# Performance work log

Measured on AMD Instinct MI355X. Metric: run time of the kernel, lower is better.

## Reference

```python
import jax, jax.numpy as jnp
import numpy as np
from jax import lax

# retina / model config (matches init_kwargs)
G, K, S = 64, 3, 2            # first patch size, n scales, scale factor
B, C, H, W = 64, 3, 512, 512  # input batch
C1, C2 = 64, 128              # feature extractor channels


def setup_inputs() -> dict:
    key = jax.random.key(0)
    k1, k2, k3, k4 = jax.random.split(key, 4)
    x = jax.random.normal(k1, (B, C, H, W), jnp.float32)
    # normalized fixation coords in [-1, 1]
    l = jax.random.uniform(k2, (B, 2), jnp.float32, minval=-1.0, maxval=1.0)
    w1 = jax.random.normal(k3, (C1, C, 3, 3), jnp.float32) * 0.05
    b1 = jnp.zeros((C1,), jnp.float32)
    w2 = jax.random.normal(k4, (C2, C1, 3, 3), jnp.float32) * 0.05
    b2 = jnp.zeros((C2,), jnp.float32)
    return {"x": x, "l": l, "w1": w1, "b1": b1, "w2": w2, "b2": b2}


def _conv(x, w, stride):
    return lax.conv_general_dilated(
        x, w, (stride, stride), 'SAME',
        dimension_numbers=('NCHW', 'OIHW', 'NCHW'))


def _extract_patches(x, coords, size):
    """Batched equivalent of crude_retina.extract_patch.

    Torch pads by size//2+1 only when the crop exceeds the image; padding
    unconditionally and offsetting the start indices yields identical values.
    x: (B,C,H,W), coords: (B,2) int [y,x]. Returns (B,C,size,size).
    """
    pad = size // 2 + 1
    xp = jnp.pad(x, ((0, 0), (0, 0), (pad, pad), (pad, pad)))
    start_y = coords[:, 0] - size // 2 + pad
    start_x = coords[:, 1] - size // 2 + pad

    def slice_one(im, sy, sx):
        return lax.dynamic_slice(im, (0, sy, sx), (im.shape[0], size, size))

    return jax.vmap(slice_one)(xp, start_y, start_x)


def _resize_nearest(p, g):
    # torch F.interpolate(mode='nearest'): src = floor(dst * in/out)
    size = p.shape[-1]
    idx = (jnp.arange(g) * size) // g
    return p[:, :, idx][:, :, :, idx]


def reference(x, l, w1, b1, w2, b2):
    T = jnp.array([H, W], jnp.float32)
    # to_exocentric: floor(0.5*(l+1)*T) clamped to [0, max(H,W)]
    coords = jnp.clip(jnp.floor(0.5 * (l + 1.0) * T), 0, max(H, W)).astype(jnp.int32)

    # multi-scale foveation
    phi = []
    size = G
    for _ in range(K):
        p = _extract_patches(x, coords, size)
        if size != G:
            p = _resize_nearest(p, G)
        phi.append(p)
        size = int(S * size)
    phi = jnp.stack(phi, axis=1)  # (B, K, C, G, G)

    # feature extractor applied per patch scale
    outs = []
    for i in range(K):
        h = jax.nn.relu(_conv(phi[:, i], w1, 1) + b1[:, None, None])
        h = jax.nn.relu(_conv(h, w2, 2) + b2[:, None, None])
        outs.append(h)
    return jnp.stack(outs, axis=1)  # (B, K, C2, G//2, G//2)
```

## Files before the change

### kernel.cpp

```cpp
#include <hip/hip_runtime.h>
#include <hip/hip_bf16.h>

typedef __attribute__((ext_vector_type(4))) float  f32x4;
typedef __attribute__((ext_vector_type(8))) _Float16 f16x8;

#define LDA1 40

static __device__ __forceinline__ void gld_lds16(const void* g, void* l) {
    __builtin_amdgcn_global_load_lds(
        (const __attribute__((address_space(1))) void*)g,
        (__attribute__((address_space(3))) void*)l, 16, 0, 0);
}

__global__ void transform_kernel(const float* __restrict__ w1, const float* __restrict__ w2,
                                 _Float16* __restrict__ Bt1, _Float16* __restrict__ Bt2)
{
    const int i = blockIdx.x * 256 + threadIdx.x;
    if (i < 64 * 32) {
        const int n = i >> 5, k = i & 31;
        const float v = (k < 27) ? w1[n * 27 + k] : 0.0f;
        Bt1[i] = (_Float16)v;
    }
    const int j = i - 64 * 32;
    if (j >= 0 && j < 9 * 128 * 64) {
        const int tap = j / (128 * 64);
        const int rem = j % (128 * 64);
        const int n = rem >> 6;
        const int c1 = rem & 63;
        Bt2[j] = (_Float16)w2[((size_t)n * 64 + c1) * 9 + tap];
    }
}

__global__ __launch_bounds__(256) void conv1_mfma(
    const float* __restrict__ x, const float* __restrict__ l,
    const _Float16* __restrict__ Bt1, const float* __restrict__ b1,
    _Float16* __restrict__ h1, int bk0)
{
    const int img = blockIdx.y;
    const int bk  = bk0 + img;
    const int b   = bk / 3, ksc = bk % 3;
    const int step = 1 << ksc;
    const int half = 32 << ksc;
    const int py0 = blockIdx.x * 4;

    const float ly = l[b * 2 + 0], lx = l[b * 2 + 1];
    int cy = (int)floorf(0.5f * (ly + 1.0f) * 512.0f);
    int cx = (int)floorf(0.5f * (lx + 1.0f) * 512.0f);
    cy = min(max(cy, 0), 512);
    cx = min(max(cx, 0), 512);
    const int sy = cy - half, sx = cx - half;

    __shared__ float    patch[3 * 6 * 66];
    __shared__ _Float16 A_lds[256 * LDA1];
    __shared__ _Float16 out_t[256 * 64];

    const int t = threadIdx.x;
    const float* xb = x + (size_t)b * 3 * 512 * 512;
    for (int i = t; i < 3 * 6 * 66; i += 256) {
        const int c  = i / 396, r = i % 396;
        const int ry = r / 66, xx = r % 66;
        const int yy = py0 - 1 + ry;
        const int col = xx - 1;
        const int iy = sy + yy * step, ix = sx + col * step;
        float v = 0.0f;
        if (yy >= 0 && yy < 64 && col >= 0 && col < 64 &&
            iy >= 0 && iy < 512 && ix >= 0 && ix < 512)
            v = xb[(size_t)c * 262144 + iy * 512 + ix];
        patch[i] = v;
    }
    __syncthreads();

    {
        const int pyl = t >> 6, px = t & 63;
        _Float16* arow = &A_lds[t * LDA1];
        #pragma unroll
        for (int k = 0; k < 27; ++k) {
            const int c = k / 9, rr = k % 9, kh = rr / 3, kw = rr % 3;
            arow[k] = (_Float16)patch[c * 396 + (pyl + kh) * 66 + (px + kw)];
        }
        #pragma unroll
        for (int k = 27; k < 32; ++k) arow[k] = (_Float16)0.0f;
    }
    __syncthreads();

    const int wave = t >> 6, lane = t & 63;
    const int lrow = lane & 15, kb = lane >> 4;

    f16x8 bfr[4];
    #pragma unroll
    for (int nf = 0; nf < 4; ++nf)
        bfr[nf] = *(const f16x8*)(Bt1 + ((size_t)(nf * 16 + lrow)) * 32 + kb * 8);

    f32x4 acc[4][4];
    #pragma unroll
    for (int mf = 0; mf < 4; ++mf)
        #pragma unroll
        for (int nf = 0; nf < 4; ++nf)
            #pragma unroll
            for (int r = 0; r < 4; ++r) acc[mf][nf][r] = 0.0f;

    #pragma unroll
    for (int mf = 0; mf < 4; ++mf) {
        const f16x8 afr = *(const f16x8*)(&A_lds[((wave * 4 + mf) * 16 + lrow) * LDA1 + kb * 8]);
        #pragma unroll
        for (int nf = 0; nf < 4; ++nf)
            acc[mf][nf] = __builtin_amdgcn_mfma_f32_16x16x32_f16(afr, bfr[nf], acc[mf][nf], 0, 0, 0);
    }

    #pragma unroll
    for (int mf = 0; mf < 4; ++mf) {
        const int ml0 = (wave * 4 + mf) * 16 + kb * 4;
        #pragma unroll
        for (int nf = 0; nf < 4; ++nf) {
            const int c1 = nf * 16 + lrow;
            const float bb = b1[c1];
            #pragma unroll
            for (int r = 0; r < 4; ++r) {
                const float v = fmaxf(acc[mf][nf][r] + bb, 0.0f);
                const int ml = ml0 + r;
                const int xcol = ml & 63;
                const int psx = ((xcol & 1) << 5) | (xcol >> 1);
                const int pl  = (ml & ~63) | psx;
                const int c1s = c1 ^ ((psx & 7) << 3);
                out_t[pl * 64 + c1s] = (_Float16)v;
            }
        }
    }
    __syncthreads();

    _Float16* hb = h1 + (size_t)img * 4096 * 64 + (size_t)py0 * 64 * 64;
    #pragma unroll
    for (int j = 0; j < 8; ++j) {
        const int idx = j * 256 + t;
        *(f16x8*)(hb + (size_t)idx * 8) = *(const f16x8*)&out_t[idx * 8];
    }
}

__global__ __launch_bounds__(256) void conv2_mfma(
    const _Float16* __restrict__ h1, const _Float16* __restrict__ Bt2,
    const float* __restrict__ b2, float* __restrict__ out, int bk0)
{
    const int img = blockIdx.y;
    const int bk  = bk0 + img;
    const int mc  = blockIdx.x;
    const int t = threadIdx.x, wave = t >> 6, lane = t & 63;
    const int lrow = lane & 15, kb = lane >> 4;
    const int wq = wave >> 1;
    const int wn = wave & 1;

    __shared__ _Float16 As[5 * 4096 + 2 * 8192];
    _Float16* Bs = As + 5 * 4096;

    const _Float16* hb = h1 + (size_t)img * 4096 * 64;
    const int ys = mc * 4;
    const int nrows = (mc == 15) ? 4 : 5;

    if (mc == 15) {
        f16x8 z = {};
        *(f16x8*)&As[4 * 4096 + t * 16]     = z;
        *(f16x8*)&As[4 * 4096 + t * 16 + 8] = z;
    }

    {
        const _Float16* ga = hb + (size_t)ys * 4096;
        #pragma unroll
        for (int j = 0; j < 10; ++j) {
            if (j < nrows * 2) {
                const int c = j * 256 + t;
                gld_lds16(ga + (size_t)c * 8, As + (j * 256 + wave * 64) * 8);
            }
        }
    }
    {
        #pragma unroll
        for (int i = 0; i < 4; ++i) {
            const int c = i * 256 + t;
            const int r = c >> 3, j = c & 7;
            const int jt = j ^ (r & 7);
            gld_lds16(Bt2 + (size_t)r * 64 + jt * 8,
                      Bs + (i * 256 + wave * 64) * 8);
        }
    }

    f32x4 acc[2][4];
    #pragma unroll
    for (int mf = 0; mf < 2; ++mf)
        #pragma unroll
        for (int nf = 0; nf < 4; ++nf)
            #pragma unroll
            for (int r = 0; r < 4; ++r) acc[mf][nf][r] = 0.0f;

    #pragma unroll 1
    for (int tap = 0; tap < 9; ++tap) {
        __syncthreads();
        if (tap < 8) {
            const _Float16* gb = Bt2 + (size_t)(tap + 1) * 8192;
            const int slot = (tap + 1) & 1;
            #pragma unroll
            for (int i = 0; i < 4; ++i) {
                const int c = i * 256 + t;
                const int r = c >> 3, j = c & 7;
                const int jt = j ^ (r & 7);
                gld_lds16(gb + (size_t)r * 64 + jt * 8,
                          Bs + slot * 8192 + (i * 256 + wave * 64) * 8);
            }
        }
        const int kh = tap / 3, kw = tap % 3;
        const int par = kw & 1;
        const int rrow = 2 * wq + kh;
        const int slot = tap & 1;

        #pragma unroll
        for (int c1h = 0; c1h < 2; ++c1h) {
            const int jt = c1h * 4 + kb;
            f16x8 afr[2];
            #pragma unroll
            for (int mf = 0; mf < 2; ++mf) {
                const int ox = mf * 16 + lrow;
                const int xh = ox + (kw >> 1);
                const int p  = rrow * 64 + par * 32 + xh;
                f16x8 v = *(const f16x8*)&As[p * 64 + (jt ^ (p & 7)) * 8];
                if ((kw == 2) && (ox == 31)) v = (f16x8){};
                afr[mf] = v;
            }
            #pragma unroll
            for (int nf = 0; nf < 4; ++nf) {
                const int r = wn * 64 + nf * 16 + lrow;
                const f16x8 bfr = *(const f16x8*)&Bs[slot * 8192 + r * 64 + (jt ^ (r & 7)) * 8];
                #pragma unroll
                for (int mf = 0; mf < 2; ++mf)
                    acc[mf][nf] = __builtin_amdgcn_mfma_f32_16x16x32_f16(afr[mf], bfr, acc[mf][nf], 0, 0, 0);
            }
        }
    }

    float* ob = out + (size_t)bk * 128 * 1024;
    #pragma unroll
    for (int mf = 0; mf < 2; ++mf) {
        const int m0 = mc * 64 + wq * 32 + mf * 16 + kb * 4;
        #pragma unroll
        for (int nf = 0; nf < 4; ++nf) {
            const int c2 = wn * 64 + nf * 16 + lrow;
            const float bb = b2[c2];
            f32x4 v;
            #pragma unroll
            for (int r = 0; r < 4; ++r) v[r] = fmaxf(acc[mf][nf][r] + bb, 0.0f);
            *(f32x4*)(ob + (size_t)c2 * 1024 + m0) = v;
        }
    }
}

extern "C" void kernel_launch(void* const* d_in, const int* in_sizes, int n_in,
                              void* d_out, int out_size, void* d_ws, size_t ws_size,
                              hipStream_t stream) {
    const float* x  = (const float*)d_in[0];
    const float* l  = (const float*)d_in[1];
    const float* w1 = (const float*)d_in[2];
    const float* b1 = (const float*)d_in[3];
    const float* w2 = (const float*)d_in[4];
    const float* b2 = (const float*)d_in[5];
    float* out = (float*)d_out;

    _Float16* Bt1 = (_Float16*)d_ws;
    _Float16* Bt2 = Bt1 + 64 * 32;
    _Float16* h1  = (_Float16*)((char*)d_ws + 160 * 1024);

    const int total_imgs = 192;
    const size_t per_img = (size_t)4096 * 64 * sizeof(_Float16);
    size_t h1_cap = (ws_size > 160 * 1024) ? ws_size - 160 * 1024 : 0;
    int ipc = (int)(h1_cap / per_img);
    if (ipc > total_imgs) ipc = total_imgs;
    if (ipc < 1) ipc = 1;

    transform_kernel<<<296, 256, 0, stream>>>(w1, w2, Bt1, Bt2);

    for (int bk0 = 0; bk0 < total_imgs; bk0 += ipc) {
        const int n = (total_imgs - bk0 < ipc) ? (total_imgs - bk0) : ipc;
        conv1_mfma<<<dim3(16, n), 256, 0, stream>>>(x, l, Bt1, b1, h1, bk0);
        conv2_mfma<<<dim3(16, n), 256, 0, stream>>>(h1, Bt2, b2, out, bk0);
    }
}
```

Measured before the change: 102.6 us.

## Gather conv1 im2col fragments directly from global into MFMA registers

Conv1 no longer stages a float patch tile and an im2col matrix in LDS. Each lane gathers its 8 K-elements straight from global memory into the B fragment, using precomputed per-lane offsets. The MFMA is also transposed so each lane's outputs are 4 consecutive channels, written as packed f16x4 stores. Each block now handles 16 rows in four sub-iterations, with a quarter as many blocks, which cuts LDS traffic and barriers but gives fewer blocks and relies on the cache for overlapping gathers.

New measurement: 111.2 us. 8.4% more time.

```diff
diff --git a/kernel.cpp b/kernel.cpp
--- a/kernel.cpp
+++ b/kernel.cpp
@@ -3,8 +3,7 @@
 
 typedef __attribute__((ext_vector_type(4))) float  f32x4;
 typedef __attribute__((ext_vector_type(8))) _Float16 f16x8;
-
-#define LDA1 40
+typedef __attribute__((ext_vector_type(4))) _Float16 f16x4;
 
 static __device__ __forceinline__ void gld_lds16(const void* g, void* l) {
     __builtin_amdgcn_global_load_lds(
@@ -41,7 +40,12 @@
     const int b   = bk / 3, ksc = bk % 3;
     const int step = 1 << ksc;
     const int half = 32 << ksc;
-    const int py0 = blockIdx.x * 4;
+    const int quarter = blockIdx.x;
+
+    const int t = threadIdx.x, wave = t >> 6, lane = t & 63;
+    const int lrow = lane & 15, kb = lane >> 4;
+
+    __shared__ _Float16 out_t[256 * 64];
 
     const float ly = l[b * 2 + 0], lx = l[b * 2 + 1];
     int cy = (int)floorf(0.5f * (ly + 1.0f) * 512.0f);
@@ -50,89 +54,73 @@
     cx = min(max(cx, 0), 512);
     const int sy = cy - half, sx = cx - half;
 
-    __shared__ float    patch[3 * 6 * 66];
-    __shared__ _Float16 A_lds[256 * LDA1];
-    __shared__ _Float16 out_t[256 * 64];
-
-    const int t = threadIdx.x;
-    const float* xb = x + (size_t)b * 3 * 512 * 512;
-    for (int i = t; i < 3 * 6 * 66; i += 256) {
-        const int c  = i / 396, r = i % 396;
-        const int ry = r / 66, xx = r % 66;
-        const int yy = py0 - 1 + ry;
-        const int col = xx - 1;
-        const int iy = sy + yy * step, ix = sx + col * step;
-        float v = 0.0f;
-        if (yy >= 0 && yy < 64 && col >= 0 && col < 64 &&
-            iy >= 0 && iy < 512 && ix >= 0 && ix < 512)
-            v = xb[(size_t)c * 262144 + iy * 512 + ix];
-        patch[i] = v;
-    }
-    __syncthreads();
-
-    {
-        const int pyl = t >> 6, px = t & 63;
-        _Float16* arow = &A_lds[t * LDA1];
-        #pragma unroll
-        for (int k = 0; k < 27; ++k) {
-            const int c = k / 9, rr = k % 9, kh = rr / 3, kw = rr % 3;
-            arow[k] = (_Float16)patch[c * 396 + (pyl + kh) * 66 + (px + kw)];
-        }
-        #pragma unroll
-        for (int k = 27; k < 32; ++k) arow[k] = (_Float16)0.0f;
-    }
-    __syncthreads();
-
-    const int wave = t >> 6, lane = t & 63;
-    const int lrow = lane & 15, kb = lane >> 4;
-
-    f16x8 bfr[4];
-    #pragma unroll
-    for (int nf = 0; nf < 4; ++nf)
-        bfr[nf] = *(const f16x8*)(Bt1 + ((size_t)(nf * 16 + lrow)) * 32 + kb * 8);
-
-    f32x4 acc[4][4];
-    #pragma unroll
-    for (int mf = 0; mf < 4; ++mf)
-        #pragma unroll
-        for (int nf = 0; nf < 4; ++nf)
-            #pragma unroll
-            for (int r = 0; r < 4; ++r) acc[mf][nf][r] = 0.0f;
-
-    #pragma unroll
-    for (int mf = 0; mf < 4; ++mf) {
-        const f16x8 afr = *(const f16x8*)(&A_lds[((wave * 4 + mf) * 16 + lrow) * LDA1 + kb * 8]);
-        #pragma unroll
-        for (int nf = 0; nf < 4; ++nf)
-            acc[mf][nf] = __builtin_amdgcn_mfma_f32_16x16x32_f16(afr, bfr[nf], acc[mf][nf], 0, 0, 0);
-    }
-
-    #pragma unroll
-    for (int mf = 0; mf < 4; ++mf) {
-        const int ml0 = (wave * 4 + mf) * 16 + kb * 4;
-        #pragma unroll
-        for (int nf = 0; nf < 4; ++nf) {
-            const int c1 = nf * 16 + lrow;
-            const float bb = b1[c1];
-            #pragma unroll
-            for (int r = 0; r < 4; ++r) {
-                const float v = fmaxf(acc[mf][nf][r] + bb, 0.0f);
-                const int ml = ml0 + r;
-                const int xcol = ml & 63;
-                const int psx = ((xcol & 1) << 5) | (xcol >> 1);
-                const int pl  = (ml & ~63) | psx;
-                const int c1s = c1 ^ ((psx & 7) << 3);
-                out_t[pl * 64 + c1s] = (_Float16)v;
-            }
-        }
-    }
-    __syncthreads();
-
-    _Float16* hb = h1 + (size_t)img * 4096 * 64 + (size_t)py0 * 64 * 64;
+    f16x8 w1f[4];
+    f32x4 b1v[4];
+    #pragma unroll
+    for (int nf = 0; nf < 4; ++nf) {
+        w1f[nf] = *(const f16x8*)(Bt1 + ((size_t)(nf * 16 + lrow)) * 32 + kb * 8);
+        b1v[nf] = *(const f32x4*)(b1 + nf * 16 + kb * 4);
+    }
+
+    const int px = wave * 16 + lrow;
+    const float* xb = x + (size_t)b * 3 * 262144;
+    int dyj[8];
+    int ixoff[8];
     #pragma unroll
     for (int j = 0; j < 8; ++j) {
-        const int idx = j * 256 + t;
-        *(f16x8*)(hb + (size_t)idx * 8) = *(const f16x8*)&out_t[idx * 8];
+        const int k   = kb * 8 + j;
+        const int c   = (k * 57) >> 9;
+        const int rem = k - c * 9;
+        const int kh  = (rem * 43) >> 7;
+        const int kw  = rem - kh * 3;
+        const int xx  = px + kw - 1;
+        const int ix  = sx + xx * step;
+        const bool xok = (k < 27) && (xx >= 0) && (xx < 64) && (ix >= 0) && (ix < 512);
+        dyj[j]   = kh - 1;
+        ixoff[j] = xok ? (c * 262144 + ix) : -1;
+    }
+
+    const int psx = ((px & 1) << 5) | (px >> 1);
+    const int c1sb = ((psx & 7) << 3);
+
+    const int py0 = quarter * 16;
+    #pragma unroll 1
+    for (int sub = 0; sub < 4; ++sub) {
+        #pragma unroll
+        for (int il = 0; il < 4; ++il) {
+            const int py  = py0 + sub * 4 + il;
+            const int iyb = sy + py * step;
+            f16x8 pfr = {};
+            #pragma unroll
+            for (int j = 0; j < 8; ++j) {
+                const int yy = py + dyj[j];
+                const int iy = iyb + dyj[j] * step;
+                float v = 0.0f;
+                if (ixoff[j] >= 0 && yy >= 0 && yy < 64 && iy >= 0 && iy < 512)
+                    v = xb[(size_t)ixoff[j] + iy * 512];
+                pfr[j] = (_Float16)v;
+            }
+            f32x4 zero = {0.0f, 0.0f, 0.0f, 0.0f};
+            #pragma unroll
+            for (int nf = 0; nf < 4; ++nf) {
+                const f32x4 d = __builtin_amdgcn_mfma_f32_16x16x32_f16(w1f[nf], pfr, zero, 0, 0, 0);
+                f16x4 hv;
+                #pragma unroll
+                for (int r = 0; r < 4; ++r)
+                    hv[r] = (_Float16)fmaxf(d[r] + b1v[nf][r], 0.0f);
+                const int c1s = (nf * 16 + kb * 4) ^ c1sb;
+                *(f16x4*)&out_t[(il * 64 + psx) * 64 + c1s] = hv;
+            }
+        }
+        __syncthreads();
+        _Float16* hb = h1 + (size_t)img * 4096 * 64
+                          + (size_t)(quarter * 1024 + sub * 256) * 64;
+        #pragma unroll
+        for (int jj = 0; jj < 8; ++jj) {
+            const int idx = jj * 256 + t;
+            *(f16x8*)(hb + (size_t)idx * 8) = *(const f16x8*)&out_t[idx * 8];
+        }
+        __syncthreads();
     }
 }
 
@@ -276,7 +264,7 @@
 
     for (int bk0 = 0; bk0 < total_imgs; bk0 += ipc) {
         const int n = (total_imgs - bk0 < ipc) ? (total_imgs - bk0) : ipc;
-        conv1_mfma<<<dim3(16, n), 256, 0, stream>>>(x, l, Bt1, b1, h1, bk0);
+        conv1_mfma<<<dim3(4, n), 256, 0, stream>>>(x, l, Bt1, b1, h1, bk0);
         conv2_mfma<<<dim3(16, n), 256, 0, stream>>>(h1, Bt2, b2, out, bk0);
     }
 }
```

## Split conv2 K-dimension into halves to shrink LDS and raise occupancy

Applied to the files above, without the earlier changes.

The conv2 MFMA kernel now stages only half of the 64 input channels at a time, with an outer loop over channel halves and the 9-tap loop inside it. The A tile is stored channel-chunk-major so the XOR swizzle is undone at load time, and the B buffers shrink to half size. LDS use drops from about 53KB to about 36KB, and a launch_bounds occupancy hint of 4 is added. The cost is re-streaming the weights twice, extra barriers, and a possible loss of the earlier swizzle's bank-conflict avoidance.

New measurement: 133.4 us. 1.3x slower.

```diff
diff --git a/kernel.cpp b/kernel.cpp
--- a/kernel.cpp
+++ b/kernel.cpp
@@ -55,7 +55,7 @@
     __shared__ _Float16 out_t[256 * 64];
 
     const int t = threadIdx.x;
-    const float* xb = x + (size_t)b * 3 * 512 * 512;
+    const float* xb = x + (size_t)b * 3 * 262144;
     for (int i = t; i < 3 * 6 * 66; i += 256) {
         const int c  = i / 396, r = i % 396;
         const int ry = r / 66, xx = r % 66;
@@ -136,7 +136,7 @@
     }
 }
 
-__global__ __launch_bounds__(256) void conv2_mfma(
+__global__ __launch_bounds__(256, 4) void conv2_mfma(
     const _Float16* __restrict__ h1, const _Float16* __restrict__ Bt2,
     const float* __restrict__ b2, float* __restrict__ out, int bk0)
 {
@@ -148,39 +148,12 @@
     const int wq = wave >> 1;
     const int wn = wave & 1;
 
-    __shared__ _Float16 As[5 * 4096 + 2 * 8192];
-    _Float16* Bs = As + 5 * 4096;
+    __shared__ _Float16 Ah[4 * 320 * 8];
+    __shared__ _Float16 Bh[2][4 * 128 * 8];
 
     const _Float16* hb = h1 + (size_t)img * 4096 * 64;
     const int ys = mc * 4;
-    const int nrows = (mc == 15) ? 4 : 5;
-
-    if (mc == 15) {
-        f16x8 z = {};
-        *(f16x8*)&As[4 * 4096 + t * 16]     = z;
-        *(f16x8*)&As[4 * 4096 + t * 16 + 8] = z;
-    }
-
-    {
-        const _Float16* ga = hb + (size_t)ys * 4096;
-        #pragma unroll
-        for (int j = 0; j < 10; ++j) {
-            if (j < nrows * 2) {
-                const int c = j * 256 + t;
-                gld_lds16(ga + (size_t)c * 8, As + (j * 256 + wave * 64) * 8);
-            }
-        }
-    }
-    {
-        #pragma unroll
-        for (int i = 0; i < 4; ++i) {
-            const int c = i * 256 + t;
-            const int r = c >> 3, j = c & 7;
-            const int jt = j ^ (r & 7);
-            gld_lds16(Bt2 + (size_t)r * 64 + jt * 8,
-                      Bs + (i * 256 + wave * 64) * 8);
-        }
-    }
+    const int nreal = ((mc == 15) ? 4 : 5) * 64;
 
     f32x4 acc[2][4];
     #pragma unroll
@@ -191,42 +164,60 @@
             for (int r = 0; r < 4; ++r) acc[mf][nf][r] = 0.0f;
 
     #pragma unroll 1
-    for (int tap = 0; tap < 9; ++tap) {
+    for (int c1h = 0; c1h < 2; ++c1h) {
         __syncthreads();
-        if (tap < 8) {
-            const _Float16* gb = Bt2 + (size_t)(tap + 1) * 8192;
-            const int slot = (tap + 1) & 1;
-            #pragma unroll
-            for (int i = 0; i < 4; ++i) {
-                const int c = i * 256 + t;
-                const int r = c >> 3, j = c & 7;
-                const int jt = j ^ (r & 7);
-                gld_lds16(gb + (size_t)r * 64 + jt * 8,
-                          Bs + slot * 8192 + (i * 256 + wave * 64) * 8);
-            }
-        }
-        const int kh = tap / 3, kw = tap % 3;
-        const int par = kw & 1;
-        const int rrow = 2 * wq + kh;
-        const int slot = tap & 1;
-
-        #pragma unroll
-        for (int c1h = 0; c1h < 2; ++c1h) {
-            const int jt = c1h * 4 + kb;
+
+        #pragma unroll
+        for (int i = 0; i < 5; ++i) {
+            const int c  = i * 256 + t;
+            const int jt = c / 320, p = c % 320;
+            if (p < nreal) {
+                const int gp = ys * 64 + p;
+                const int cs = (c1h * 32 + jt * 8) ^ ((gp & 7) << 3);
+                gld_lds16(hb + (size_t)gp * 64 + cs, Ah + (size_t)c * 8);
+            } else {
+                *(f16x8*)&Ah[(size_t)c * 8] = (f16x8){};
+            }
+        }
+        #pragma unroll
+        for (int i = 0; i < 2; ++i) {
+            const int c  = i * 256 + t;
+            const int jt = c >> 7, r = c & 127;
+            gld_lds16(Bt2 + (size_t)r * 64 + c1h * 32 + jt * 8, &Bh[0][c * 8]);
+        }
+
+        #pragma unroll 1
+        for (int tap = 0; tap < 9; ++tap) {
+            __syncthreads();
+            if (tap < 8) {
+                const int slot = (tap + 1) & 1;
+                #pragma unroll
+                for (int i = 0; i < 2; ++i) {
+                    const int c  = i * 256 + t;
+                    const int jt = c >> 7, r = c & 127;
+                    gld_lds16(Bt2 + (size_t)(tap + 1) * 8192 + r * 64 + c1h * 32 + jt * 8,
+                              &Bh[slot][c * 8]);
+                }
+            }
+            const int kh = tap / 3, kw = tap % 3;
+            const int par = kw & 1;
+            const int rrow = 2 * wq + kh;
+            const int slot = tap & 1;
+
             f16x8 afr[2];
             #pragma unroll
             for (int mf = 0; mf < 2; ++mf) {
                 const int ox = mf * 16 + lrow;
                 const int xh = ox + (kw >> 1);
                 const int p  = rrow * 64 + par * 32 + xh;
-                f16x8 v = *(const f16x8*)&As[p * 64 + (jt ^ (p & 7)) * 8];
+                f16x8 v = *(const f16x8*)&Ah[(kb * 320 + p) * 8];
                 if ((kw == 2) && (ox == 31)) v = (f16x8){};
                 afr[mf] = v;
             }
             #pragma unroll
             for (int nf = 0; nf < 4; ++nf) {
                 const int r = wn * 64 + nf * 16 + lrow;
-                const f16x8 bfr = *(const f16x8*)&Bs[slot * 8192 + r * 64 + (jt ^ (r & 7)) * 8];
+                const f16x8 bfr = *(const f16x8*)&Bh[slot][(kb * 128 + r) * 8];
                 #pragma unroll
                 for (int mf = 0; mf < 2; ++mf)
                     acc[mf][nf] = __builtin_amdgcn_mfma_f32_16x16x32_f16(afr[mf], bfr, acc[mf][nf], 0, 0, 0);
```
